# Kernel tuning notes

Hardware: AMD Instinct MI355X
Metric: run time of the kernel (lower is better)

## Reference

```python
import jax, jax.numpy as jnp
import numpy as np

B, S = 512, 512
M, DK, DV, DF = 64, 128, 256, 128
NQ = 10000

def setup_inputs() -> dict:
    key = jax.random.key(0)
    ks = jax.random.split(key, 20)
    g = lambda i, sh, sc: jax.random.normal(ks[i], sh, jnp.float32) * sc
    return {
        'q_data': jax.random.randint(ks[0], (B, S), 0, NQ + 1),
        'qa_data': jax.random.randint(ks[1], (B, S), 0, 2 * NQ + 1),
        'target': jax.random.uniform(ks[2], (B * S, 1), jnp.float32),  # all >= 0 -> mask all valid
        'q_embed_w': g(3, (NQ + 1, DK), 0.1),
        'qa_embed_w': g(4, (2 * NQ + 1, DV), 0.1),
        'key_mem': g(5, (M, DK), 0.1),
        'init_value_mem': g(6, (M, DV), 0.1),
        'erase_w': g(7, (DV, DV), 0.05), 'erase_b': jnp.zeros((DV,), jnp.float32),
        'add_w': g(8, (DV, DV), 0.05), 'add_b': jnp.zeros((DV,), jnp.float32),
        'input_w': g(9, (DF, DK), 0.05), 'input_b': jnp.zeros((DF,), jnp.float32),
        'read_w': g(10, (DF, DV + DF), 0.05), 'read_b': jnp.zeros((DF,), jnp.float32),
        'predict_w': g(11, (1, DF), 0.05), 'predict_b': jnp.zeros((1,), jnp.float32),
    }


def reference(q_data, qa_data, target, q_embed_w, qa_embed_w, key_mem, init_value_mem,
              erase_w, erase_b, add_w, add_b, input_w, input_b, read_w, read_b,
              predict_w, predict_b):
    q_e = q_embed_w[q_data]      # [B,S,DK]
    qa_e = qa_embed_w[qa_data]   # [B,S,DV]

    def step(Mv, inp):
        q, qa = inp                                       # [B,DK], [B,DV]
        w = jax.nn.softmax(q @ key_mem.T, axis=-1)        # [B,M]
        read = jnp.einsum('bm,bmd->bd', w, Mv)            # [B,DV]
        erase = jax.nn.sigmoid(qa @ erase_w.T + erase_b)  # [B,DV]
        add = jnp.tanh(qa @ add_w.T + add_b)              # [B,DV]
        Mv = Mv * (1.0 - w[:, :, None] * erase[:, None, :]) + w[:, :, None] * add[:, None, :]
        return Mv, read

    Mv0 = jnp.broadcast_to(init_value_mem, (q_data.shape[0], M, DV))
    _, reads = jax.lax.scan(step, Mv0, (q_e.transpose(1, 0, 2), qa_e.transpose(1, 0, 2)))
    reads = reads.transpose(1, 0, 2)                       # [B,S,DV]

    ie = jnp.tanh(q_e @ input_w.T + input_b)               # [B,S,DF]
    rce = jnp.tanh(jnp.concatenate([reads, ie], axis=-1) @ read_w.T + read_b)
    pred = rce @ predict_w.T + predict_b                   # [B,S,1]
    pred_logit = jax.nn.sigmoid(pred)

    pred_1d = pred.reshape(-1)
    t = target.reshape(-1)
    mask = t >= 0.0
    # stable BCE-with-logits, masked mean (mask is all-True with this setup)
    bce = jnp.maximum(pred_1d, 0.0) - pred_1d * t + jnp.log1p(jnp.exp(-jnp.abs(pred_1d)))
    denom = jnp.maximum(jnp.sum(mask.astype(jnp.float32)), 1.0)
    loss = jnp.sum(jnp.where(mask, bce, 0.0)) / denom
    filtered_pred = jax.nn.sigmoid(jnp.where(mask, pred_1d, 0.0))
    filtered_target = jnp.where(mask, t, 0.0)
    return pred_logit, loss, filtered_pred, filtered_target
```

## Files before the change

### kernel.cpp

```cpp
#include <hip/hip_runtime.h>
#include <hip/hip_bf16.h>
#include <math.h>

#define BB 512
#define SS 512
#define MM 64
#define DK 128
#define DV 256
#define DF 128
#define CHUNK 16
#define NCHUNK (SS/CHUNK)

typedef __attribute__((ext_vector_type(8))) short s8v;
typedef __attribute__((ext_vector_type(4))) float f4v;
typedef __attribute__((ext_vector_type(2))) float f2v;
typedef __attribute__((ext_vector_type(8))) unsigned short u16x8;

#define MFMA16(a,b,c) __builtin_amdgcn_mfma_f32_16x16x32_bf16((a),(b),(c),0,0,0)

#define EAP_OFF 0
#define KTP_OFF 131072
#define ITP_OFF 139264
#define RTP_OFF 155648
#define WTAB_BYTE 409664
#define IET_BYTE  2969920
#define EAT_BYTE  5530176
#define WS_NEED2  26011200ull
#define READS_BYTE 26011264ull
#define WS_NEED3  (READS_BYTE + (size_t)BB*SS*DV*2)
#define PART_STRIDE_B 32768

__device__ __forceinline__ unsigned short f2bf(float x) {
    union { float f; unsigned u; } v; v.f = x;
    unsigned r = v.u + 0x7fffu + ((v.u >> 16) & 1u);
    return (unsigned short)(r >> 16);
}
__device__ __forceinline__ float bf2f(unsigned short h) {
    union { unsigned u; float f; } v; v.u = ((unsigned)h) << 16;
    return v.f;
}
__device__ __forceinline__ float u2f(unsigned u) {
    union { unsigned x; float f; } v; v.x = u; return v.f;
}
__device__ __forceinline__ float sigmoidf_(float x) { return 1.0f / (1.0f + __expf(-x)); }
__device__ __forceinline__ float fast_tanh(float x) {
    float e = __expf(2.0f * x);
    return 1.0f - 2.0f / (e + 1.0f);
}

__global__ void prep_kernel(const float* __restrict__ ew, const float* __restrict__ aw,
                            const float* __restrict__ km, const float* __restrict__ iw,
                            const float* __restrict__ rw, float* __restrict__ wsf) {
    int tid = blockIdx.x * 256 + threadIdx.x;
    int stride = gridDim.x * 256;
    if (tid < 2) wsf[tid] = 0.0f;
    unsigned short* bp = (unsigned short*)(wsf + 16);

    for (int i = tid; i < 131072; i += stride) {
        int e = i & 7, l = (i >> 3) & 63, ks = (i >> 9) & 7, nf = i >> 12;
        int k = ks*32 + (l >> 4)*8 + e;
        int n = nf*16 + (l & 15);
        float v = (n < 256) ? ew[n*DV + k] : aw[(n-256)*DV + k];
        bp[EAP_OFF + i] = f2bf(v);
    }
    for (int i = tid; i < 8192; i += stride) {
        int e = i & 7, l = (i >> 3) & 63, ks = (i >> 9) & 3, nf = i >> 11;
        int k = ks*32 + (l >> 4)*8 + e;
        int m = nf*16 + (l & 15);
        bp[KTP_OFF + i] = f2bf(km[m*DK + k]);
    }
    for (int i = tid; i < 16384; i += stride) {
        int e = i & 7, l = (i >> 3) & 63, ks = (i >> 9) & 3, nf = i >> 11;
        int k = ks*32 + (l >> 4)*8 + e;
        int f = nf*16 + (l & 15);
        bp[ITP_OFF + i] = f2bf(iw[f*DK + k]);
    }
    for (int i = tid; i < 49152; i += stride) {
        int e = i & 7, l = (i >> 3) & 63, g = i >> 9;
        int ks = g % 12, nf = g / 12;
        int j = ks*32 + (l >> 4)*8 + e;
        int f = nf*16 + (l & 15);
        bp[RTP_OFF + i] = f2bf(rw[f*(DV+DF) + j]);
    }
}

__launch_bounds__(256, 2)
__global__ void table_kernel(const float* __restrict__ q_embed, const float* __restrict__ qa_embed,
                             const float* __restrict__ erase_b, const float* __restrict__ add_b,
                             const float* __restrict__ input_b, const float* __restrict__ read_b,
                             int rw2flag, float* __restrict__ ws) {
    __shared__ __align__(128) char tsm[65536];
    const int tid  = threadIdx.x;
    const int lane = tid & 63;
    const int wave = tid >> 6;
    const int arow = lane & 15;
    const int ag   = lane >> 4;

    const unsigned short* wsb = (const unsigned short*)(ws + 16);
    const s8v* eap = (const s8v*)(wsb + EAP_OFF);
    const s8v* ktp = (const s8v*)(wsb + KTP_OFF);
    const s8v* itp = (const s8v*)(wsb + ITP_OFF);
    const s8v* rtp = (const s8v*)(wsb + RTP_OFF);
    float*          wtab = (float*)((char*)ws + WTAB_BYTE);
    unsigned short* iet  = (unsigned short*)((char*)ws + IET_BYTE);
    unsigned short* eat  = (unsigned short*)((char*)ws + EAT_BYTE);

    if (blockIdx.x < 157) {
        const int r0 = blockIdx.x * 64;
        char*  q16   = tsm;
        float* sc    = (float*)(tsm + 16384);
        unsigned short* iest = (unsigned short*)(tsm + 33792);

        #pragma unroll
        for (int it = 0; it < 8; ++it) {
            int u = it*256 + tid;
            int row = u >> 5, c4 = u & 31;
            int sr = r0 + row; if (sr > 10000) sr = 10000;
            float4 v = *(const float4*)(q_embed + sr*DK + c4*4);
            ushort4 p; p.x = f2bf(v.x); p.y = f2bf(v.y); p.z = f2bf(v.z); p.w = f2bf(v.w);
            *(ushort4*)(q16 + ((row*256 + c4*8) ^ ((row & 7) << 4))) = p;
        }
        __syncthreads();

        {
            s8v a[4];
            #pragma unroll
            for (int ks = 0; ks < 4; ++ks)
                a[ks] = *(const s8v*)(q16 + (((wave*16+arow)*256 + ks*64 + ag*16) ^ ((arow & 7) << 4)));
            #pragma unroll
            for (int j = 0; j < 4; ++j) {
                f4v cc = {0.f,0.f,0.f,0.f};
                #pragma unroll
                for (int ks = 0; ks < 4; ++ks) cc = MFMA16(a[ks], ktp[(j*4 + ks)*64 + lane], cc);
                #pragma unroll
                for (int r = 0; r < 4; ++r)
                    sc[(wave*16 + ag*4 + r)*68 + j*16 + arow] = cc[r];
            }
            __syncthreads();

            #pragma unroll
            for (int k = 0; k < 16; ++k) {
                int rr = wave*16 + k;
                float v = sc[rr*68 + lane];
                float mx = v;
                #pragma unroll
                for (int off = 32; off; off >>= 1) mx = fmaxf(mx, __shfl_xor(mx, off));
                float e = __expf(v - mx);
                float sum = e;
                #pragma unroll
                for (int off = 32; off; off >>= 1) sum += __shfl_xor(sum, off);
                if (r0 + rr < 10001) wtab[(r0 + rr)*64 + lane] = e / sum;
            }

            #pragma unroll
            for (int j = 0; j < 8; ++j) {
                f4v cc = {0.f,0.f,0.f,0.f};
                #pragma unroll
                for (int ks = 0; ks < 4; ++ks) cc = MFMA16(a[ks], itp[(j*4 + ks)*64 + lane], cc);
                float bias = input_b[j*16 + arow];
                #pragma unroll
                for (int r = 0; r < 4; ++r)
                    iest[(wave*16 + ag*4 + r)*128 + j*16 + arow] = f2bf(fast_tanh(cc[r] + bias));
            }
        }
        __syncthreads();

        if (rw2flag) {
            s8v af2[4];
            #pragma unroll
            for (int ks2 = 0; ks2 < 4; ++ks2)
                af2[ks2] = *(const s8v*)((const char*)iest + (wave*16+arow)*256 + ks2*64 + ag*16);
            f4v acc2[8];
            #pragma unroll
            for (int j = 0; j < 8; ++j) acc2[j] = (f4v){0.f,0.f,0.f,0.f};
            #pragma unroll
            for (int ks2 = 0; ks2 < 4; ++ks2)
                #pragma unroll
                for (int j = 0; j < 8; ++j)
                    acc2[j] = MFMA16(af2[ks2], rtp[(j*12 + 8 + ks2)*64 + lane], acc2[j]);
            #pragma unroll
            for (int j = 0; j < 8; ++j) {
                float rb = read_b[j*16 + arow];
                #pragma unroll
                for (int r = 0; r < 4; ++r)
                    iest[(wave*16 + ag*4 + r)*128 + j*16 + arow] = f2bf(acc2[j][r] + rb);
            }
            __syncthreads();
        }
        #pragma unroll
        for (int it = 0; it < 4; ++it) {
            int u = it*256 + tid;
            int row = u >> 4, c8 = u & 15;
            if (r0 + row < 10001)
                *(u16x8*)(iet + (r0 + row)*128 + c8*8) = *(const u16x8*)(iest + row*128 + c8*8);
        }
    } else {
        const int r0 = (blockIdx.x - 157) * 64;
        char* qa16 = tsm;
        unsigned short* east = (unsigned short*)(tsm + 32768);

        #pragma unroll
        for (int it = 0; it < 16; ++it) {
            int u = it*256 + tid;
            int row = u >> 6, c4 = u & 63;
            int sr = r0 + row; if (sr > 20000) sr = 20000;
            float4 v = *(const float4*)(qa_embed + sr*DV + c4*4);
            ushort4 p; p.x = f2bf(v.x); p.y = f2bf(v.y); p.z = f2bf(v.z); p.w = f2bf(v.w);
            *(ushort4*)(qa16 + ((row*512 + c4*8) ^ ((row & 7) << 4))) = p;
        }
        __syncthreads();

        s8v af[8];
        #pragma unroll
        for (int ks = 0; ks < 8; ++ks)
            af[ks] = *(const s8v*)(qa16 + (((wave*16+arow)*512 + ks*64 + ag*16) ^ ((arow & 7) << 4)));

        for (int h = 0; h < 2; ++h) {
            #pragma unroll
            for (int i = 0; i < 16; ++i) {
                int nt = h*16 + i;
                f4v cc = {0.f,0.f,0.f,0.f};
                #pragma unroll
                for (int ks = 0; ks < 8; ++ks) cc = MFMA16(af[ks], eap[(nt*8 + ks)*64 + lane], cc);
                int n = nt*16 + arow;
                float bias = (n < 256) ? erase_b[n] : add_b[n - 256];
                #pragma unroll
                for (int r = 0; r < 4; ++r) {
                    float v = cc[r] + bias;
                    float res = (n < 256) ? sigmoidf_(v) : fast_tanh(v);
                    east[(wave*16 + ag*4 + r)*256 + (n - h*256)] = f2bf(res);
                }
            }
            __syncthreads();
            #pragma unroll
            for (int it = 0; it < 8; ++it) {
                int u = it*256 + tid;
                int row = u >> 5, c8 = u & 31;
                if (r0 + row < 20001)
                    *(u16x8*)(eat + (size_t)(r0 + row)*512 + h*256 + c8*8) =
                        *(const u16x8*)(east + row*256 + c8*8);
            }
            __syncthreads();
        }
    }
}

__launch_bounds__(256, 4)
__global__ void scan2_kernel(const int* __restrict__ q_data, const int* __restrict__ qa_data,
                             const float* __restrict__ init_mv,
                             float* __restrict__ ws) {
    __shared__ float          wf [CHUNK][68];
    __shared__ unsigned       eaL[CHUNK][68];
    __shared__ unsigned short rdp[CHUNK][4][68];

    const int bid = blockIdx.x;
    const int xcd = bid & 7, idx = bid >> 3;
    const int b   = xcd*64 + (idx >> 2);
    const int dq  = idx & 3;
    const int tid = threadIdx.x;
    const int d   = tid & 63;
    const int mq  = tid >> 6;

    const float*          wtab  = (const float*)((const char*)ws + WTAB_BYTE);
    const unsigned short* eat   = (const unsigned short*)((const char*)ws + EAT_BYTE);
    unsigned short*       reads = (unsigned short*)((char*)ws + READS_BYTE);

    f2v mv2[8];
    #pragma unroll
    for (int j = 0; j < 8; ++j) {
        mv2[j][0] = init_mv[(mq*16 + 2*j    )*DV + dq*64 + d];
        mv2[j][1] = init_mv[(mq*16 + 2*j + 1)*DV + dq*64 + d];
    }

    const int base = b * SS;
    const bool eaRole = (tid < 128);
    const int erow = tid >> 3;
    const int eu   = tid & 7;
    const int wrow = (tid - 128) >> 3;
    const int wu   = tid & 7;

    int ia0, iq0, ia1, iq1;
    u16x8 per, pad_; float4 pw0, pw1;

    auto loadidx = [&](int cc, int& xa, int& xq) {
        if (eaRole) xa = qa_data[base + cc*CHUNK + erow];
        else        xq = q_data [base + cc*CHUNK + wrow];
    };
    auto loadrows = [&]() {
        if (eaRole) {
            per  = *(const u16x8*)(eat + (size_t)ia0*512 +       dq*64 + eu*8);
            pad_ = *(const u16x8*)(eat + (size_t)ia0*512 + 256 + dq*64 + eu*8);
        } else {
            pw0 = *(const float4*)(wtab + iq0*64 + wu*8);
            pw1 = *(const float4*)(wtab + iq0*64 + wu*8 + 4);
        }
    };
    auto storerows = [&]() {
        if (eaRole) {
            unsigned pk[8];
            #pragma unroll
            for (int i = 0; i < 8; ++i)
                pk[i] = (unsigned)per[i] | ((unsigned)pad_[i] << 16);
            *(uint4*)&eaL[erow][eu*8]     = *(uint4*)&pk[0];
            *(uint4*)&eaL[erow][eu*8 + 4] = *(uint4*)&pk[4];
        } else {
            *(float4*)&wf[wrow][wu*8]     = pw0;
            *(float4*)&wf[wrow][wu*8 + 4] = pw1;
        }
    };

    loadidx(0, ia0, iq0);
    loadrows();
    loadidx(1, ia1, iq1);

    for (int c = 0; c < NCHUNK; ++c) {
        storerows();
        __syncthreads();
        ia0 = ia1; iq0 = iq1;
        if (c + 1 < NCHUNK) loadrows();
        { int c2 = (c + 2 < NCHUNK) ? c + 2 : NCHUNK - 1; loadidx(c2, ia1, iq1); }

        #pragma unroll
        for (int s = 0; s < CHUNK; ++s) {
            unsigned eac = eaL[s][d];
            float e = u2f(eac << 16);
            float a = u2f(eac & 0xffff0000u);
            f2v e2; e2[0] = e; e2[1] = e;
            f2v a2; a2[0] = a; a2[1] = a;
            const f2v* wr = (const f2v*)&wf[s][mq*16];
            f2v r0 = {0.f, 0.f}, r1 = {0.f, 0.f};
            #pragma unroll
            for (int j = 0; j < 8; j += 2) {
                f2v w0 = wr[j], w1 = wr[j+1];
                r0 = __builtin_elementwise_fma(w0, mv2[j], r0);
                mv2[j] = __builtin_elementwise_fma(
                    w0, __builtin_elementwise_fma(-mv2[j], e2, a2), mv2[j]);
                r1 = __builtin_elementwise_fma(w1, mv2[j+1], r1);
                mv2[j+1] = __builtin_elementwise_fma(
                    w1, __builtin_elementwise_fma(-mv2[j+1], e2, a2), mv2[j+1]);
            }
            f2v rs = r0 + r1;
            rdp[s][mq][d] = f2bf(rs[0] + rs[1]);
        }
        __syncthreads();

        {
            int s = tid >> 4, d0 = (tid & 15) * 4;
            float a0 = 0.f, a1 = 0.f, a2 = 0.f, a3 = 0.f;
            #pragma unroll
            for (int m2 = 0; m2 < 4; ++m2) {
                ushort4 v = *(const ushort4*)&rdp[s][m2][d0];
                a0 += bf2f(v.x); a1 += bf2f(v.y); a2 += bf2f(v.z); a3 += bf2f(v.w);
            }
            ushort4 o; o.x = f2bf(a0); o.y = f2bf(a1); o.z = f2bf(a2); o.w = f2bf(a3);
            *(ushort4*)(reads + (size_t)(base + c*CHUNK + s)*DV + dq*64 + d0) = o;
        }
    }
}

__launch_bounds__(256, 2)
__global__ void rce_kernel(const int* __restrict__ q_data, const float* __restrict__ target,
                           const float* __restrict__ predict_w, const float* __restrict__ predict_b,
                           float* __restrict__ ws, float* __restrict__ out) {
    __shared__ __align__(128) char cat16[33792];
    __shared__ __align__(16) unsigned short rw2s[64][128];
    __shared__ float lred[4][2];
    float* rce_f = (float*)cat16;

    const int blk  = blockIdx.x;
    const int b    = blk >> 3;
    const int s0   = (blk & 7) * 64;
    const int tid  = threadIdx.x;
    const int lane = tid & 63;
    const int wave = tid >> 6;
    const int arow = lane & 15;
    const int ag   = lane >> 4;

    const unsigned short* wsb   = (const unsigned short*)(ws + 16);
    const s8v*            rtp   = (const s8v*)(wsb + RTP_OFF);
    const unsigned short* rw2t  = (const unsigned short*)((const char*)ws + IET_BYTE);
    const unsigned short* reads = (const unsigned short*)((const char*)ws + READS_BYTE);

    #pragma unroll
    for (int it = 0; it < 8; ++it) {
        int u = it*256 + tid, row = u >> 5, cu = u & 31;
        u16x8 v = *(const u16x8*)(reads + (size_t)(b*SS + s0 + row)*DV + cu*8);
        *(u16x8*)(cat16 + ((row*512 + cu*16) ^ ((row & 7) << 4))) = v;
    }
    #pragma unroll
    for (int it = 0; it < 4; ++it) {
        int u = it*256 + tid, row = u >> 4, cu = u & 15;
        int iq = q_data[b*SS + s0 + row];
        *(u16x8*)(&rw2s[row][cu*8]) = *(const u16x8*)(rw2t + (size_t)iq*128 + cu*8);
    }
    __syncthreads();

    f4v acc[8];
    #pragma unroll
    for (int n = 0; n < 8; ++n) acc[n] = (f4v){0.f,0.f,0.f,0.f};
    #pragma unroll
    for (int ks = 0; ks < 8; ++ks) {
        int row = wave*16 + arow;
        s8v a = *(const s8v*)(cat16 + ((row*512 + ks*64 + ag*16) ^ ((row & 7) << 4)));
        #pragma unroll
        for (int n = 0; n < 8; ++n)
            acc[n] = MFMA16(a, rtp[(n*12 + ks)*64 + lane], acc[n]);
    }
    __syncthreads();

    #pragma unroll
    for (int n = 0; n < 8; ++n) {
        #pragma unroll
        for (int r = 0; r < 4; ++r) {
            int rr = wave*16 + ag*4 + r, col = n*16 + arow;
            rce_f[rr*132 + col] = fast_tanh(acc[n][r] + bf2f(rw2s[rr][col]));
        }
    }
    __syncthreads();

    const float pw_lo = predict_w[lane];
    const float pw_hi = predict_w[lane + 64];
    float local_loss = 0.f, local_cnt = 0.f;
    #pragma unroll
    for (int k = 0; k < 16; ++k) {
        int r = wave*16 + k;
        float p = fmaf(pw_lo, rce_f[r*132 + lane], pw_hi * rce_f[r*132 + 64 + lane]);
        #pragma unroll
        for (int off = 32; off; off >>= 1) p += __shfl_xor(p, off);
        if (lane == 0) {
            p += predict_b[0];
            int gi = b*SS + s0 + r;
            float t = target[gi];
            bool mask = t >= 0.0f;
            out[gi] = sigmoidf_(p);
            out[BB*SS + 1 + gi] = sigmoidf_(mask ? p : 0.0f);
            out[2*BB*SS + 1 + gi] = mask ? t : 0.0f;
            if (mask) {
                local_loss += fmaxf(p, 0.0f) - p*t + log1pf(__expf(-fabsf(p)));
                local_cnt  += 1.0f;
            }
        }
    }
    if (lane == 0) { lred[wave][0] = local_loss; lred[wave][1] = local_cnt; }
    __syncthreads();
    if (tid == 0) {
        float L = lred[0][0] + lred[1][0] + lred[2][0] + lred[3][0];
        float C = lred[0][1] + lred[1][1] + lred[2][1] + lred[3][1];
        float* part = (float*)((char*)ws + READS_BYTE + (size_t)blk * PART_STRIDE_B);
        part[0] = L; part[1] = C;
    }
}

__global__ void finish_kernel(float* __restrict__ ws, float* __restrict__ out, int mode) {
    if (mode == 0) {
        if (threadIdx.x == 0) out[BB*SS] = ws[0] / fmaxf(ws[1], 1.0f);
        return;
    }
    __shared__ float sl[4][2];
    const int tid = threadIdx.x, lane = tid & 63, wave = tid >> 6;
    const char* base = (const char*)ws + READS_BYTE;
    float L = 0.f, C = 0.f;
    for (int i = tid; i < 4096; i += 256) {
        const float* p = (const float*)(base + (size_t)i * PART_STRIDE_B);
        L += p[0]; C += p[1];
    }
    #pragma unroll
    for (int off = 32; off; off >>= 1) {
        L += __shfl_xor(L, off);
        C += __shfl_xor(C, off);
    }
    if (lane == 0) { sl[wave][0] = L; sl[wave][1] = C; }
    __syncthreads();
    if (tid == 0) {
        float LL = sl[0][0] + sl[1][0] + sl[2][0] + sl[3][0];
        float CC = sl[0][1] + sl[1][1] + sl[2][1] + sl[3][1];
        out[BB*SS] = LL / fmaxf(CC, 1.0f);
    }
}

__launch_bounds__(512, 2)
__global__ void scan_kernel(const int* __restrict__ q_data, const int* __restrict__ qa_data,
                            const float* __restrict__ target,
                            const float* __restrict__ init_mv,
                            const float* __restrict__ read_b,
                            const float* __restrict__ predict_w, const float* __restrict__ predict_b,
                            float* __restrict__ ws, float* __restrict__ out) {
    __shared__ __align__(128) char smem[50176];
    char*           cat16 = smem;
    float*          wf    = (float*)(smem + 12288);
    unsigned short* eaL   = (unsigned short*)(smem + 16640);
    unsigned short* rdp   = (unsigned short*)(smem + 33280);
    float*          rce_f = (float*)(smem + 41728);

    const int b    = blockIdx.x;
    const int tid  = threadIdx.x;
    const int lane = tid & 63;
    const int wave = tid >> 6;
    const int arow = lane & 15;
    const int ag   = lane >> 4;
    const int d    = tid & 255;
    const int half = tid >> 8;

    const unsigned short* wsb = (const unsigned short*)(ws + 16);
    const s8v* rtp = (const s8v*)(wsb + RTP_OFF);
    const float*          wtab = (const float*)((const char*)ws + WTAB_BYTE);
    const unsigned short* iet  = (const unsigned short*)((const char*)ws + IET_BYTE);
    const unsigned short* eat  = (const unsigned short*)((const char*)ws + EAT_BYTE);

    float mv[32];
    #pragma unroll
    for (int i = 0; i < 32; ++i) mv[i] = init_mv[(half*32 + i)*DV + d];

    const float rb    = read_b[wave*16 + arow];
    const float pw_lo = predict_w[lane];
    const float pw_hi = predict_w[lane + 64];

    const int base  = b * SS;
    const int erow  = tid >> 5;
    const int eunit = tid & 31;
    const int role  = tid >> 8;
    const int grow  = (tid >> 4) & 15;
    const int gunit = tid & 15;

    int iqa0, iq0, iqa1, iq1;
    u16x8 pe0, pe1, pie;
    float4 pwf;

    auto loadidx = [&](int cc, int& xa, int& xq) {
        xa = qa_data[base + cc*CHUNK + erow];
        xq = q_data [base + cc*CHUNK + grow];
    };
    auto loadrows = [&]() {
        const unsigned short* er_ptr = eat + (size_t)iqa0*512 + eunit*16;
        pe0 = *(const u16x8*)(er_ptr);
        pe1 = *(const u16x8*)(er_ptr + 8);
        if (role == 0) pwf = *(const float4*)(wtab + iq0*64 + gunit*4);
        else           pie = *(const u16x8*)(iet + (size_t)iq0*128 + gunit*8);
    };
    auto storerows = [&]() {
        *(u16x8*)(eaL + erow*520 + eunit*16)     = pe0;
        *(u16x8*)(eaL + erow*520 + eunit*16 + 8) = pe1;
        if (role == 0) *(float4*)((char*)wf + grow*272 + gunit*16) = pwf;
        else *(u16x8*)(cat16 + ((grow*768 + 512 + gunit*16) ^ ((grow & 7) << 4))) = pie;
    };

    loadidx(0, iqa0, iq0);
    loadrows();
    loadidx(1, iqa1, iq1);

    float local_loss = 0.0f, local_cnt = 0.0f;

    for (int c = 0; c < NCHUNK; ++c) {
        storerows();
        __syncthreads();
        iqa0 = iqa1; iq0 = iq1;
        if (c + 1 < NCHUNK) loadrows();
        { int c2 = (c + 2 < NCHUNK) ? c + 2 : NCHUNK - 1; loadidx(c2, iqa1, iq1); }

        for (int s = 0; s < CHUNK; ++s) {
            float e = bf2f(eaL[s*520 + d]);
            float a = bf2f(eaL[s*520 + 256 + d]);
            const float4* wr4 = (const float4*)(wf + s*68 + half*32);
            float r0 = 0.f, r1 = 0.f, r2 = 0.f, r3 = 0.f;
            #pragma unroll
            for (int j = 0; j < 8; ++j) {
                float4 w = wr4[j];
                r0 = fmaf(w.x, mv[j*4+0], r0); mv[j*4+0] = fmaf(w.x, fmaf(-mv[j*4+0], e, a), mv[j*4+0]);
                r1 = fmaf(w.y, mv[j*4+1], r1); mv[j*4+1] = fmaf(w.y, fmaf(-mv[j*4+1], e, a), mv[j*4+1]);
                r2 = fmaf(w.z, mv[j*4+2], r2); mv[j*4+2] = fmaf(w.z, fmaf(-mv[j*4+2], e, a), mv[j*4+2]);
                r3 = fmaf(w.w, mv[j*4+3], r3); mv[j*4+3] = fmaf(w.w, fmaf(-mv[j*4+3], e, a), mv[j*4+3]);
            }
            float rd = (r0 + r1) + (r2 + r3);
            if (half == 0) {
                *(unsigned short*)(cat16 + ((s*768 + d*2) ^ ((s & 7) << 4))) = f2bf(rd);
            } else {
                rdp[s*264 + d] = f2bf(rd);
            }
        }
        __syncthreads();

        if (half == 0) {
            #pragma unroll
            for (int s = 0; s < CHUNK; ++s) {
                unsigned short* p = (unsigned short*)(cat16 + ((s*768 + d*2) ^ ((s & 7) << 4)));
                *p = f2bf(bf2f(*p) + bf2f(rdp[s*264 + d]));
            }
        }
        __syncthreads();

        {
            f4v cc = {0.f,0.f,0.f,0.f};
            #pragma unroll
            for (int ks = 0; ks < 12; ++ks) {
                s8v a = *(const s8v*)(cat16 + ((arow*768 + ks*64 + ag*16) ^ ((arow & 7) << 4)));
                cc = MFMA16(a, rtp[(wave*12 + ks)*64 + lane], cc);
            }
            #pragma unroll
            for (int r = 0; r < 4; ++r)
                rce_f[(ag*4 + r)*132 + wave*16 + arow] = fast_tanh(cc[r] + rb);
        }
        __syncthreads();

        #pragma unroll
        for (int k = 0; k < 2; ++k) {
            int r = wave*2 + k;
            float p = fmaf(pw_lo, rce_f[r*132 + lane], pw_hi * rce_f[r*132 + 64 + lane]);
            #pragma unroll
            for (int off = 32; off; off >>= 1) p += __shfl_xor(p, off);
            if (lane == 0) {
                p += predict_b[0];
                int gi = b*SS + c*CHUNK + r;
                float t = target[gi];
                bool mask = t >= 0.0f;
                out[gi] = sigmoidf_(p);
                float pm = mask ? p : 0.0f;
                out[BB*SS + 1 + gi] = sigmoidf_(pm);
                out[2*BB*SS + 1 + gi] = mask ? t : 0.0f;
                if (mask) {
                    local_loss += fmaxf(p, 0.0f) - p*t + log1pf(__expf(-fabsf(p)));
                    local_cnt  += 1.0f;
                }
            }
        }
    }

    #pragma unroll
    for (int off = 32; off; off >>= 1) {
        local_loss += __shfl_xor(local_loss, off);
        local_cnt  += __shfl_xor(local_cnt, off);
    }
    if (lane == 0) {
        atomicAdd(&ws[0], local_loss);
        atomicAdd(&ws[1], local_cnt);
    }
}

extern "C" void kernel_launch(void* const* d_in, const int* in_sizes, int n_in,
                              void* d_out, int out_size, void* d_ws, size_t ws_size,
                              hipStream_t stream) {
    const int*   q_data    = (const int*)d_in[0];
    const int*   qa_data   = (const int*)d_in[1];
    const float* target    = (const float*)d_in[2];
    const float* q_embed   = (const float*)d_in[3];
    const float* qa_embed  = (const float*)d_in[4];
    const float* key_mem   = (const float*)d_in[5];
    const float* init_mv   = (const float*)d_in[6];
    const float* erase_w   = (const float*)d_in[7];
    const float* erase_b   = (const float*)d_in[8];
    const float* add_w     = (const float*)d_in[9];
    const float* add_b     = (const float*)d_in[10];
    const float* input_w   = (const float*)d_in[11];
    const float* input_b   = (const float*)d_in[12];
    const float* read_w    = (const float*)d_in[13];
    const float* read_b    = (const float*)d_in[14];
    const float* predict_w = (const float*)d_in[15];
    const float* predict_b = (const float*)d_in[16];

    float* ws  = (float*)d_ws;
    float* out = (float*)d_out;

    hipLaunchKernelGGL(prep_kernel, dim3(256), dim3(256), 0, stream,
                       erase_w, add_w, key_mem, input_w, read_w, ws);
    if (ws_size >= WS_NEED3) {
        hipLaunchKernelGGL(table_kernel, dim3(470), dim3(256), 0, stream,
                           q_embed, qa_embed, erase_b, add_b, input_b, read_b, 1, ws);
        hipLaunchKernelGGL(scan2_kernel, dim3(2048), dim3(256), 0, stream,
                           q_data, qa_data, init_mv, ws);
        hipLaunchKernelGGL(rce_kernel, dim3(4096), dim3(256), 0, stream,
                           q_data, target, predict_w, predict_b, ws, out);
        hipLaunchKernelGGL(finish_kernel, dim3(1), dim3(256), 0, stream, ws, out, 1);
    } else {
        hipLaunchKernelGGL(table_kernel, dim3(470), dim3(256), 0, stream,
                           q_embed, qa_embed, erase_b, add_b, input_b, read_b, 0, ws);
        hipLaunchKernelGGL(scan_kernel, dim3(BB), dim3(512), 0, stream,
                           q_data, qa_data, target, init_mv,
                           read_b, predict_w, predict_b, ws, out);
        hipLaunchKernelGGL(finish_kernel, dim3(1), dim3(256), 0, stream, ws, out, 0);
    }
}
```

Baseline: 527.4 us.

## Interleave erase/add table and load per-thread directly in scan, use inline pk_fma

Changes the erase/add table layout to interleaved 32-bit pairs (erase low, add high) written straight from MFMA results, dropping the LDS staging pass in the prep kernel when rw2flag is set. The scan kernel no longer stages erase/add rows through shared memory; each thread loads its own packed value per step from global memory, and the w-table loading is simplified to one float4 per thread. The inner update uses inline-asm v_pk_fma_f32 with neg modifiers so the compiler emits packed FMAs. The risk is more scattered global loads inside the serial scan loop, adding latency, and the scan now depends on rw2flag being set for the layout to match.

```diff
diff --git a/kernel.cpp b/kernel.cpp
--- a/kernel.cpp
+++ b/kernel.cpp
@@ -47,6 +47,15 @@
     float e = __expf(2.0f * x);
     return 1.0f - 2.0f / (e + 1.0f);
 }
+__device__ __forceinline__ void pk_fma_acc(f2v& acc, f2v a, f2v b) {
+    asm("v_pk_fma_f32 %0, %1, %2, %0" : "+v"(acc) : "v"(a), "v"(b));
+}
+__device__ __forceinline__ f2v pk_nfma(f2v a, f2v b, f2v c) {
+    f2v d;
+    asm("v_pk_fma_f32 %0, %1, %2, %3 neg_lo:[1,0,0] neg_hi:[1,0,0]"
+        : "=v"(d) : "v"(a), "v"(b), "v"(c));
+    return d;
+}
 
 __global__ void prep_kernel(const float* __restrict__ ew, const float* __restrict__ aw,
                             const float* __restrict__ km, const float* __restrict__ iw,
@@ -104,6 +113,7 @@
     float*          wtab = (float*)((char*)ws + WTAB_BYTE);
     unsigned short* iet  = (unsigned short*)((char*)ws + IET_BYTE);
     unsigned short* eat  = (unsigned short*)((char*)ws + EAT_BYTE);
+    unsigned*       eat2 = (unsigned*)((char*)ws + EAT_BYTE);
 
     if (blockIdx.x < 157) {
         const int r0 = blockIdx.x * 64;
@@ -197,7 +207,6 @@
     } else {
         const int r0 = (blockIdx.x - 157) * 64;
         char* qa16 = tsm;
-        unsigned short* east = (unsigned short*)(tsm + 32768);
 
         #pragma unroll
         for (int it = 0; it < 16; ++it) {
@@ -215,32 +224,54 @@
         for (int ks = 0; ks < 8; ++ks)
             af[ks] = *(const s8v*)(qa16 + (((wave*16+arow)*512 + ks*64 + ag*16) ^ ((arow & 7) << 4)));
 
-        for (int h = 0; h < 2; ++h) {
+        if (rw2flag) {
             #pragma unroll
             for (int i = 0; i < 16; ++i) {
-                int nt = h*16 + i;
-                f4v cc = {0.f,0.f,0.f,0.f};
-                #pragma unroll
-                for (int ks = 0; ks < 8; ++ks) cc = MFMA16(af[ks], eap[(nt*8 + ks)*64 + lane], cc);
-                int n = nt*16 + arow;
-                float bias = (n < 256) ? erase_b[n] : add_b[n - 256];
+                f4v ce = {0.f,0.f,0.f,0.f}, ca = {0.f,0.f,0.f,0.f};
+                #pragma unroll
+                for (int ks = 0; ks < 8; ++ks) {
+                    ce = MFMA16(af[ks], eap[((i     )*8 + ks)*64 + lane], ce);
+                    ca = MFMA16(af[ks], eap[((i + 16)*8 + ks)*64 + lane], ca);
+                }
+                int n = i*16 + arow;
+                float eb = erase_b[n], ab = add_b[n];
                 #pragma unroll
                 for (int r = 0; r < 4; ++r) {
-                    float v = cc[r] + bias;
-                    float res = (n < 256) ? sigmoidf_(v) : fast_tanh(v);
-                    east[(wave*16 + ag*4 + r)*256 + (n - h*256)] = f2bf(res);
+                    int row = r0 + wave*16 + ag*4 + r;
+                    unsigned u = (unsigned)f2bf(sigmoidf_(ce[r] + eb))
+                               | ((unsigned)f2bf(fast_tanh(ca[r] + ab)) << 16);
+                    if (row < 20001) eat2[(size_t)row*256 + n] = u;
                 }
             }
-            __syncthreads();
-            #pragma unroll
-            for (int it = 0; it < 8; ++it) {
-                int u = it*256 + tid;
-                int row = u >> 5, c8 = u & 31;
-                if (r0 + row < 20001)
-                    *(u16x8*)(eat + (size_t)(r0 + row)*512 + h*256 + c8*8) =
-                        *(const u16x8*)(east + row*256 + c8*8);
-            }
-            __syncthreads();
+        } else {
+            unsigned short* east = (unsigned short*)(tsm + 32768);
+            for (int h = 0; h < 2; ++h) {
+                #pragma unroll
+                for (int i = 0; i < 16; ++i) {
+                    int nt = h*16 + i;
+                    f4v cc = {0.f,0.f,0.f,0.f};
+                    #pragma unroll
+                    for (int ks = 0; ks < 8; ++ks) cc = MFMA16(af[ks], eap[(nt*8 + ks)*64 + lane], cc);
+                    int n = nt*16 + arow;
+                    float bias = (n < 256) ? erase_b[n] : add_b[n - 256];
+                    #pragma unroll
+                    for (int r = 0; r < 4; ++r) {
+                        float v = cc[r] + bias;
+                        float res = (n < 256) ? sigmoidf_(v) : fast_tanh(v);
+                        east[(wave*16 + ag*4 + r)*256 + (n - h*256)] = f2bf(res);
+                    }
+                }
+                __syncthreads();
+                #pragma unroll
+                for (int it = 0; it < 8; ++it) {
+                    int u = it*256 + tid;
+                    int row = u >> 5, c8 = u & 31;
+                    if (r0 + row < 20001)
+                        *(u16x8*)(eat + (size_t)(r0 + row)*512 + h*256 + c8*8) =
+                            *(const u16x8*)(east + row*256 + c8*8);
+                }
+                __syncthreads();
+            }
         }
     }
 }
@@ -250,7 +281,6 @@
                              const float* __restrict__ init_mv,
                              float* __restrict__ ws) {
     __shared__ float          wf [CHUNK][68];
-    __shared__ unsigned       eaL[CHUNK][68];
     __shared__ unsigned short rdp[CHUNK][4][68];
 
     const int bid = blockIdx.x;
@@ -261,9 +291,9 @@
     const int d   = tid & 63;
     const int mq  = tid >> 6;
 
-    const float*          wtab  = (const float*)((const char*)ws + WTAB_BYTE);
-    const unsigned short* eat   = (const unsigned short*)((const char*)ws + EAT_BYTE);
-    unsigned short*       reads = (unsigned short*)((char*)ws + READS_BYTE);
+    const float*    wtab  = (const float*)((const char*)ws + WTAB_BYTE);
+    const unsigned* eat2  = (const unsigned*)((const char*)ws + EAT_BYTE);
+    unsigned short* reads = (unsigned short*)((char*)ws + READS_BYTE);
 
     f2v mv2[8];
     #pragma unroll
@@ -273,56 +303,33 @@
     }
 
     const int base = b * SS;
-    const bool eaRole = (tid < 128);
-    const int erow = tid >> 3;
-    const int eu   = tid & 7;
-    const int wrow = (tid - 128) >> 3;
-    const int wu   = tid & 7;
-
-    int ia0, iq0, ia1, iq1;
-    u16x8 per, pad_; float4 pw0, pw1;
-
-    auto loadidx = [&](int cc, int& xa, int& xq) {
-        if (eaRole) xa = qa_data[base + cc*CHUNK + erow];
-        else        xq = q_data [base + cc*CHUNK + wrow];
-    };
-    auto loadrows = [&]() {
-        if (eaRole) {
-            per  = *(const u16x8*)(eat + (size_t)ia0*512 +       dq*64 + eu*8);
-            pad_ = *(const u16x8*)(eat + (size_t)ia0*512 + 256 + dq*64 + eu*8);
-        } else {
-            pw0 = *(const float4*)(wtab + iq0*64 + wu*8);
-            pw1 = *(const float4*)(wtab + iq0*64 + wu*8 + 4);
-        }
-    };
-    auto storerows = [&]() {
-        if (eaRole) {
-            unsigned pk[8];
-            #pragma unroll
-            for (int i = 0; i < 8; ++i)
-                pk[i] = (unsigned)per[i] | ((unsigned)pad_[i] << 16);
-            *(uint4*)&eaL[erow][eu*8]     = *(uint4*)&pk[0];
-            *(uint4*)&eaL[erow][eu*8 + 4] = *(uint4*)&pk[4];
-        } else {
-            *(float4*)&wf[wrow][wu*8]     = pw0;
-            *(float4*)&wf[wrow][wu*8 + 4] = pw1;
-        }
-    };
-
-    loadidx(0, ia0, iq0);
-    loadrows();
-    loadidx(1, ia1, iq1);
+    const int ead  = dq*64 + d;
+    const int srow = tid >> 4;
+    const int wu   = tid & 15;
+
+    int iq0, iq1;
+    float4 pw;
+    iq0 = q_data[base + srow];
+    pw  = *(const float4*)(wtab + (size_t)iq0*64 + wu*4);
+    iq1 = q_data[base + CHUNK + srow];
 
     for (int c = 0; c < NCHUNK; ++c) {
-        storerows();
-        __syncthreads();
-        ia0 = ia1; iq0 = iq1;
-        if (c + 1 < NCHUNK) loadrows();
-        { int c2 = (c + 2 < NCHUNK) ? c + 2 : NCHUNK - 1; loadidx(c2, ia1, iq1); }
-
+        *(float4*)&wf[srow][wu*4] = pw;
+        __syncthreads();
+        iq0 = iq1;
+        if (c + 1 < NCHUNK) pw = *(const float4*)(wtab + (size_t)iq0*64 + wu*4);
+        { int c2 = (c + 2 < NCHUNK) ? c + 2 : NCHUNK - 1; iq1 = q_data[base + c2*CHUNK + srow]; }
+
+        unsigned ea[CHUNK];
         #pragma unroll
         for (int s = 0; s < CHUNK; ++s) {
-            unsigned eac = eaL[s][d];
+            int ias = qa_data[base + c*CHUNK + s];
+            ea[s] = eat2[(size_t)ias*256 + ead];
+        }
+
+        #pragma unroll
+        for (int s = 0; s < CHUNK; ++s) {
+            unsigned eac = ea[s];
             float e = u2f(eac << 16);
             float a = u2f(eac & 0xffff0000u);
             f2v e2; e2[0] = e; e2[1] = e;
@@ -332,12 +339,12 @@
             #pragma unroll
             for (int j = 0; j < 8; j += 2) {
                 f2v w0 = wr[j], w1 = wr[j+1];
-                r0 = __builtin_elementwise_fma(w0, mv2[j], r0);
-                mv2[j] = __builtin_elementwise_fma(
-                    w0, __builtin_elementwise_fma(-mv2[j], e2, a2), mv2[j]);
-                r1 = __builtin_elementwise_fma(w1, mv2[j+1], r1);
-                mv2[j+1] = __builtin_elementwise_fma(
-                    w1, __builtin_elementwise_fma(-mv2[j+1], e2, a2), mv2[j+1]);
+                pk_fma_acc(r0, w0, mv2[j]);
+                f2v t0 = pk_nfma(mv2[j], e2, a2);
+                pk_fma_acc(mv2[j], w0, t0);
+                pk_fma_acc(r1, w1, mv2[j+1]);
+                f2v t1 = pk_nfma(mv2[j+1], e2, a2);
+                pk_fma_acc(mv2[j+1], w1, t1);
             }
             f2v rs = r0 + r1;
             rdp[s][mq][d] = f2bf(rs[0] + rs[1]);
```

Measured after the change: 565.7 us. 7.3% more time.
